# Performance work log

Measured on AMD Instinct MI355X. Metric: run time of the kernel, lower is better.

Reference implementation:

```python
import jax, jax.numpy as jnp
import numpy as np

N, E = 50000, 1600000
D_IN, D_OUT = 256, 64
ALPHA = 0.2        # LeakyReLU slope used on attention logits (self.leakyrelu)
BT_SLOPE = 0.01    # F.leaky_relu default slope inside relu_bt


def _xavier_normal(key, shape, gain):
    fan_in, fan_out = shape[0], shape[1]
    std = gain * np.sqrt(2.0 / (fan_in + fan_out))
    return jax.random.normal(key, shape, dtype=jnp.float32) * std


def relu_bt(x):
    # -threshold(-leaky_relu(x), -t, -t) == min(leaky_relu(x), t), t = ||x||_inf (detached)
    t = jax.lax.stop_gradient(jnp.max(jnp.abs(x)))
    y = jnp.where(x >= 0, x, BT_SLOPE * x)
    return jnp.minimum(y, t)


def setup_inputs() -> dict:
    key = jax.random.key(0)
    k0, k1, k2, k3, k4, k5 = jax.random.split(key, 6)
    inp = jax.random.normal(k0, (N, D_IN), dtype=jnp.float32)
    edge = jax.random.randint(k1, (2, E), 0, N, dtype=jnp.int64)
    W_high = _xavier_normal(k2, (D_IN, D_OUT), 1.414)
    W_low = _xavier_normal(k3, (D_IN, D_OUT), 1.414)
    a_high = _xavier_normal(k4, (1, D_OUT), 1.414)
    a_low = _xavier_normal(k5, (1, D_OUT), 1.414)
    return {"input": inp, "edge": edge, "W_high": W_high, "W_low": W_low,
            "a_high": a_high, "a_low": a_low}


def reference(input, edge, W_high, W_low, a_high, a_low):
    n = input.shape[0]
    src, dst = edge[0], edge[1]

    h_high = relu_bt(input @ W_high)  # [N, D_OUT]
    h_low = relu_bt(input @ W_low)    # [N, D_OUT]

    # a @ (h[src] -/+ h[dst])^T == (a.h)[src] -/+ (a.h)[dst]: compute per-node scalar
    # projections first, then gather scalars per edge (avoids [E, D_OUT] edge features).
    s_high = h_high @ a_high[0]       # [N]
    s_low = h_low @ a_low[0]          # [N]

    def lrelu(x):
        return jnp.where(x >= 0, x, ALPHA * x)

    edge_e_high = jnp.exp(-lrelu(s_high[src] - s_high[dst]))  # [E]
    edge_e_low = jnp.exp(-lrelu(s_low[src] + s_low[dst]))     # [E]
    # dropout p=0.0 -> identity

    # sparse A @ ones -> per-row sum of attention weights
    rowsum_high = jax.ops.segment_sum(edge_e_high, src, num_segments=n)[:, None]
    rowsum_low = jax.ops.segment_sum(edge_e_low, src, num_segments=n)[:, None]

    # sparse A @ h -> weighted aggregation of neighbor features
    hp_high = jax.ops.segment_sum(edge_e_high[:, None] * h_high[dst], src, num_segments=n)
    hp_low = jax.ops.segment_sum(edge_e_low[:, None] * h_low[dst], src, num_segments=n)

    hp_high = hp_high / (rowsum_high + 1e-16)
    hp_low = hp_low / (rowsum_low + 1e-16)

    # concat=True branch
    return relu_bt(jnp.concatenate([hp_high, hp_low], axis=1))  # [N, 2*D_OUT]
```

## Files before the change

### kernel.cpp

```cpp
#include <hip/hip_runtime.h>
#include <hip/hip_bf16.h>
#include <cstdint>

#define NN    50000
#define NE    1600000
#define DIN   256
#define DOUT  64
#define CAPS  96
#define CAPD  95

#define BKT   196
#define BCAP  10240
#define EPB   4096
#define EPT   16
#define NBIN  391
#define MTB   64
#define NGEMM 782
#define CSPL  4

typedef __attribute__((ext_vector_type(8))) short frag8;
typedef __attribute__((ext_vector_type(4))) float fragc;

union PK { __hip_bfloat162 b2; uint32_t u; };
union CH { frag8 v; uint32_t u[4]; };

__device__ __forceinline__ float leaky01(float x) { return x >= 0.f ? x : 0.01f * x; }

__device__ __forceinline__ uint32_t pk2(float lo, float hi) {
  PK p; p.b2 = __float22bfloat162_rn(make_float2(lo, hi)); return p.u;
}

__device__ __forceinline__ int   bcast_i(int v, int lane) {
  return __builtin_amdgcn_readlane(v, lane);
}
__device__ __forceinline__ float bcast_f(float v, int lane) {
  return __int_as_float(__builtin_amdgcn_readlane(__float_as_int(v), lane));
}

__device__ __forceinline__ float bfH(uint32_t u) { return __uint_as_float(u << 16); }
__device__ __forceinline__ float bfL(uint32_t u) { return __uint_as_float(u & 0xffff0000u); }

__global__ __launch_bounds__(256) void prep_kernel(
    const float* __restrict__ Wh, const float* __restrict__ Wl,
    __hip_bfloat16* __restrict__ Wt, int* __restrict__ cursor)
{
  if (blockIdx.x == 0 && threadIdx.x < BKT) cursor[threadIdx.x] = 0;
  int g = blockIdx.x * 256 + threadIdx.x;
  if (g < 2 * DOUT * DIN) {
    int m = g >> 14, rem = g & 16383;
    int n = rem >> 8, k = rem & 255;
    float v = (m ? Wl : Wh)[k * DOUT + n];
    Wt[g] = __float2bfloat16(v);
  }
}

__global__ __launch_bounds__(256) void fused_kernel(
    const float* __restrict__ inp, const __hip_bfloat16* __restrict__ Wt,
    const float* __restrict__ ah, const float* __restrict__ al,
    const int* __restrict__ edge, int* __restrict__ cursor,
    uint32_t* __restrict__ binned, uint32_t* __restrict__ HL,
    float2* __restrict__ ss)
{
  __shared__ __align__(16) char smem[32768];

  const int idx = blockIdx.x;
  const int t = threadIdx.x;

  if (idx < NBIN) {
    uint32_t* stage  = (uint32_t*)smem;
    int*      hist   = (int*)(smem + 16384);
    int*      cur    = (int*)(smem + 17408);
    int*      base_g = (int*)(smem + 18192);
    int*      scan_s = (int*)(smem + 18976);

    const int e0 = idx * EPB;
    uint32_t v[EPT];
#pragma unroll
    for (int i = 0; i < EPT; i++) {
      int e = e0 + i * 256 + t;
      if (e < NE) {
        uint32_t s = (uint32_t)edge[e];
        uint32_t d = (uint32_t)edge[NE + e];
        v[i] = (s << 16) | d;
      } else {
        v[i] = 0xFFFFFFFFu;
      }
    }
    if (t < 256) hist[t] = 0;
    for (int b = t; b < BKT; b += 256) cur[b] = 0;
    __syncthreads();
#pragma unroll
    for (int i = 0; i < EPT; i++) {
      int b = v[i] >> 24;
      if (b < BKT) atomicAdd(&hist[b], 1);
    }
    __syncthreads();
    if (t < 64) {
      int carry = 0;
#pragma unroll
      for (int seg = 0; seg < 4; seg++) {
        int i = seg * 64 + t;
        int h = hist[i];
        int s = h;
#pragma unroll
        for (int off = 1; off < 64; off <<= 1) {
          int o = __shfl_up(s, off);
          if (t >= off) s += o;
        }
        int excl = carry + s - h;
        if (i <= BKT) scan_s[i] = excl;
        carry += bcast_i(s, 63);
      }
    }
    __syncthreads();
    for (int b = t; b < BKT; b += 256) {
      int h = hist[b];
      base_g[b] = h ? atomicAdd(&cursor[b], h) : 0;
    }
    __syncthreads();
#pragma unroll
    for (int i = 0; i < EPT; i++) {
      int b = v[i] >> 24;
      if (b < BKT) {
        int pos = atomicAdd(&cur[b], 1);
        stage[scan_s[b] + pos] = v[i];
      }
    }
    __syncthreads();
    const int total = scan_s[BKT];
    for (int i = t; i < total; i += 256) {
      uint32_t sv = stage[i];
      int bb = sv >> 24;
      int ofs = base_g[bb] + (i - scan_s[bb]);
      if (ofs < BCAP) binned[(size_t)bb * BCAP + ofs] = sv;
    }
    return;
  }

  frag8* asmem = (frag8*)smem;
  const int gid = idx - NBIN;
  const int n0 = gid * MTB;
  const int lane = t & 63;
  const int w = t >> 6;
  const int quad = lane >> 4, nn = lane & 15;

  const frag8* Wt8 = (const frag8*)Wt;
  const int bbase = ((w * 16 + nn) << 5) + quad;
  frag8 bH[8], bL[8];
#pragma unroll
  for (int q = 0; q < 8; q++) {
    bH[q] = Wt8[bbase + (q << 2)];
    bL[q] = Wt8[2048 + bbase + (q << 2)];
  }

  const float4* inp4 = (const float4*)inp;
#pragma unroll
  for (int i = 0; i < 8; i++) {
    int c = i * 256 + t;
    int r = c & 15;
    int cc = c >> 4;
    int qd = cc & 3;
    int wq = cc >> 2;
    int row = ((wq >> 3) << 4) + r;
    int k0 = ((wq & 7) << 5) + (qd << 3);
    int node = n0 + row;
    float4 a0 = make_float4(0.f, 0.f, 0.f, 0.f), a1 = a0;
    if (node < NN) {
      a0 = inp4[(size_t)node * 64 + (k0 >> 2)];
      a1 = inp4[(size_t)node * 64 + (k0 >> 2) + 1];
    }
    CH ch;
    ch.u[0] = pk2(a0.x, a0.y);
    ch.u[1] = pk2(a0.z, a0.w);
    ch.u[2] = pk2(a1.x, a1.y);
    ch.u[3] = pk2(a1.z, a1.w);
    asmem[c] = ch.v;
  }
  __syncthreads();

  fragc accH[4], accL[4];
#pragma unroll
  for (int m = 0; m < 4; m++) {
    accH[m] = (fragc){0.f, 0.f, 0.f, 0.f};
    accL[m] = (fragc){0.f, 0.f, 0.f, 0.f};
  }

#pragma unroll
  for (int q = 0; q < 8; q++) {
#pragma unroll
    for (int mt = 0; mt < 4; mt++) {
      frag8 af = asmem[(mt << 9) + (q << 6) + lane];
      accH[mt] = __builtin_amdgcn_mfma_f32_16x16x32_bf16(af, bH[q], accH[mt], 0, 0, 0);
      accL[mt] = __builtin_amdgcn_mfma_f32_16x16x32_bf16(af, bL[q], accL[mt], 0, 0, 0);
    }
  }
  __syncthreads();

  float* sred = (float*)smem;
  const float ahv = ah[w * 16 + nn];
  const float alv = al[w * 16 + nn];
#pragma unroll
  for (int mt = 0; mt < 4; mt++) {
#pragma unroll
    for (int r = 0; r < 4; r++) {
      int rowb = (mt << 4) + (quad << 2) + r;
      int node = n0 + rowb;
      float hH = leaky01(accH[mt][r]);
      float hL = leaky01(accL[mt][r]);
      if (node < NN) HL[(size_t)node * DOUT + w * 16 + nn] = pk2(hH, hL);
      float pH = hH * ahv, pL = hL * alv;
#pragma unroll
      for (int off = 1; off < 16; off <<= 1) {
        pH += __shfl_xor(pH, off);
        pL += __shfl_xor(pL, off);
      }
      if (nn == 0) {
        sred[rowb * 8 + w]     = pH;
        sred[rowb * 8 + 4 + w] = pL;
      }
    }
  }
  __syncthreads();
  if (t < 64) {
    int node = n0 + t;
    if (node < NN) {
      float sH = sred[t * 8 + 0] + sred[t * 8 + 1] + sred[t * 8 + 2] + sred[t * 8 + 3];
      float sL = sred[t * 8 + 4] + sred[t * 8 + 5] + sred[t * 8 + 6] + sred[t * 8 + 7];
      ss[node] = make_float2(sH, sL);
    }
  }
}

__global__ __launch_bounds__(256) void csr_kernel(
    const uint32_t* __restrict__ binned, const int* __restrict__ cursor,
    int* __restrict__ col)
{
  __shared__ int lst[64][CAPS];
  __shared__ int cnt[64];
  const int b    = blockIdx.x / CSPL;
  const int part = blockIdx.x % CSPL;
  const int t = threadIdx.x;
  if (t < 64) cnt[t] = 0;
  __syncthreads();
  int n = cursor[b]; if (n > BCAP) n = BCAP;
  const uint32_t* eb = binned + (size_t)b * BCAP;
  for (int i = t; i < n; i += 256) {
    uint32_t v = eb[i];
    int src = v >> 16, dst = v & 0xffff;
    int loc = src & 255;
    if ((loc >> 6) == part) {
      int pos = atomicAdd(&cnt[loc & 63], 1);
      if (pos < CAPD) lst[loc & 63][1 + pos] = dst;
    }
  }
  __syncthreads();
  if (t < 64) {
    int c = cnt[t]; if (c > CAPD) c = CAPD;
    lst[t][0] = c;
  }
  __syncthreads();
  const int base_node = (b << 8) + (part << 6);
  int4* dst4 = (int4*)(col + (size_t)base_node * CAPS);
  const int4* src4 = (const int4*)&lst[0][0];
  for (int i = t; i < 64 * CAPS / 4; i += 256) {
    int node = base_node + i / (CAPS / 4);
    if (node < NN) dst4[i] = src4[i];
  }
}

__global__ __launch_bounds__(256) void agg_kernel(
    const uint32_t* __restrict__ HL, const float2* __restrict__ ss,
    const int* __restrict__ col, float* __restrict__ out)
{
  int wave = (blockIdx.x * blockDim.x + threadIdx.x) >> 6;
  int lane = threadIdx.x & 63;
  if (wave >= NN) return;
  const int n = wave;
  const int* cl = col + (size_t)n * CAPS;
  int d = cl[0]; if (d > CAPD) d = CAPD;

  const float2 sn = ss[n];

  float accH = 0.f, accL = 0.f, rsH = 0.f, rsL = 0.f;

  for (int base = 0; base < d; base += 64) {
    int m = d - base; if (m > 64) m = 64;
    int   dst_l = 0;
    float eh_l = 0.f, el_l = 0.f;
    if (lane < m) {
      dst_l = cl[1 + base + lane];
      float2 sd = ss[dst_l];
      float xh = sn.x - sd.x;
      xh = (xh >= 0.f) ? xh : 0.2f * xh;
      eh_l = __expf(-xh);
      float xl = sn.y + sd.y;
      xl = (xl >= 0.f) ? xl : 0.2f * xl;
      el_l = __expf(-xl);
    }
    int j = 0;
    for (; j + 8 <= m; j += 8) {
      uint32_t u[8]; float eh[8], el[8];
#pragma unroll
      for (int x = 0; x < 8; x++) {
        int dd = bcast_i(dst_l, j + x);
        u[x]  = HL[((uint32_t)dd << 6) + lane];
        eh[x] = bcast_f(eh_l, j + x);
        el[x] = bcast_f(el_l, j + x);
      }
#pragma unroll
      for (int x = 0; x < 8; x++) {
        accH += eh[x] * bfH(u[x]); accL += el[x] * bfL(u[x]);
        rsH += eh[x]; rsL += el[x];
      }
    }
    for (; j < m; j++) {
      int      dst = bcast_i(dst_l, j);
      float    eh  = bcast_f(eh_l, j);
      float    el  = bcast_f(el_l, j);
      uint32_t u   = HL[((uint32_t)dst << 6) + lane];
      accH += eh * bfH(u);
      accL += el * bfL(u);
      rsH += eh;
      rsL += el;
    }
  }

  float oh = accH / (rsH + 1e-16f);
  float ol = accL / (rsL + 1e-16f);
  out[(size_t)n * 128 + lane]      = leaky01(oh);
  out[(size_t)n * 128 + 64 + lane] = leaky01(ol);
}

extern "C" void kernel_launch(void* const* d_in, const int* in_sizes, int n_in,
                              void* d_out, int out_size, void* d_ws, size_t ws_size,
                              hipStream_t stream) {
  const float* inp  = (const float*)d_in[0];
  const int*   edge = (const int*)d_in[1];
  const float* Wh   = (const float*)d_in[2];
  const float* Wl   = (const float*)d_in[3];
  const float* ah   = (const float*)d_in[4];
  const float* al   = (const float*)d_in[5];
  float* out = (float*)d_out;

  char* ws = (char*)d_ws;
  uint32_t* HL     = (uint32_t*)(ws + 0);
  float2*   ss     = (float2*)  (ws + 12800000);
  int*      col    = (int*)     (ws + 13200000);
  uint32_t* binned = (uint32_t*)(ws + 32400000);
  int*      cursor = (int*)     (ws + 40428160);
  __hip_bfloat16* Wt = (__hip_bfloat16*)(ws + 13200000);

  prep_kernel<<<128, 256, 0, stream>>>(Wh, Wl, Wt, cursor);
  fused_kernel<<<NBIN + NGEMM, 256, 0, stream>>>(inp, Wt, ah, al, edge,
                                                 cursor, binned, HL, ss);
  csr_kernel<<<BKT * CSPL, 256, 0, stream>>>(binned, cursor, col);
  agg_kernel<<<NN / 4, 256, 0, stream>>>(HL, ss, col, out);
}
```

Baseline: 198.0 us.

## Split agg wave into half-waves gathering two edges per step with 8-byte loads

The aggregation loop now has each half of the wave handle a different neighbour edge at the same time: the lower half takes even edges, the upper half takes odd edges. Each lane loads a uint2 of packed bf16 features, so a half-wave covers a full 64-column row. Edge indices and weights are broadcast with ds_bpermute instead of readlane. Row sums are computed with a butterfly shuffle reduction rather than per-edge accumulation, and the two halves' partial sums are combined with a final xor-32 shuffle before a float2 store. The aim is to halve the serial gather iterations and widen each memory request, at the cost of extra cross-lane shuffles and some wasted slots when the degree is small.

```diff
diff --git a/kernel.cpp b/kernel.cpp
--- a/kernel.cpp
+++ b/kernel.cpp
@@ -32,9 +32,6 @@
 
 __device__ __forceinline__ int   bcast_i(int v, int lane) {
   return __builtin_amdgcn_readlane(v, lane);
-}
-__device__ __forceinline__ float bcast_f(float v, int lane) {
-  return __int_as_float(__builtin_amdgcn_readlane(__float_as_int(v), lane));
 }
 
 __device__ __forceinline__ float bfH(uint32_t u) { return __uint_as_float(u << 16); }
@@ -280,8 +277,13 @@
   int d = cl[0]; if (d > CAPD) d = CAPD;
 
   const float2 sn = ss[n];
-
-  float accH = 0.f, accL = 0.f, rsH = 0.f, rsL = 0.f;
+  const uint2* HL2 = (const uint2*)HL;
+
+  const int vodd4 = (lane & 32) >> 3;
+  const int lo31  = lane & 31;
+
+  float accH0 = 0.f, accH1 = 0.f, accL0 = 0.f, accL1 = 0.f;
+  float rsH = 0.f, rsL = 0.f;
 
   for (int base = 0; base < d; base += 64) {
     int m = d - base; if (m > 64) m = 64;
@@ -297,38 +299,51 @@
       xl = (xl >= 0.f) ? xl : 0.2f * xl;
       el_l = __expf(-xl);
     }
-    int j = 0;
-    for (; j + 8 <= m; j += 8) {
-      uint32_t u[8]; float eh[8], el[8];
-#pragma unroll
-      for (int x = 0; x < 8; x++) {
-        int dd = bcast_i(dst_l, j + x);
-        u[x]  = HL[((uint32_t)dd << 6) + lane];
-        eh[x] = bcast_f(eh_l, j + x);
-        el[x] = bcast_f(el_l, j + x);
-      }
-#pragma unroll
-      for (int x = 0; x < 8; x++) {
-        accH += eh[x] * bfH(u[x]); accL += el[x] * bfL(u[x]);
-        rsH += eh[x]; rsL += el[x];
-      }
-    }
-    for (; j < m; j++) {
-      int      dst = bcast_i(dst_l, j);
-      float    eh  = bcast_f(eh_l, j);
-      float    el  = bcast_f(el_l, j);
-      uint32_t u   = HL[((uint32_t)dst << 6) + lane];
-      accH += eh * bfH(u);
-      accL += el * bfL(u);
-      rsH += eh;
-      rsL += el;
-    }
-  }
-
-  float oh = accH / (rsH + 1e-16f);
-  float ol = accL / (rsL + 1e-16f);
-  out[(size_t)n * 128 + lane]      = leaky01(oh);
-  out[(size_t)n * 128 + 64 + lane] = leaky01(ol);
+    const int ehb = __float_as_int(eh_l);
+    const int elb = __float_as_int(el_l);
+    const int pj = (m + 1) >> 1;
+    for (int jj = 0; jj < pj; jj += 4) {
+      int vdd[4]; float veh[4], vel[4]; uint2 u[4];
+#pragma unroll
+      for (int x = 0; x < 4; x++) {
+        int ib = vodd4 + ((jj + x) << 3);
+        vdd[x] = __builtin_amdgcn_ds_bpermute(ib, dst_l);
+        veh[x] = __int_as_float(__builtin_amdgcn_ds_bpermute(ib, ehb));
+        vel[x] = __int_as_float(__builtin_amdgcn_ds_bpermute(ib, elb));
+      }
+#pragma unroll
+      for (int x = 0; x < 4; x++)
+        u[x] = HL2[(((uint32_t)vdd[x]) << 5) + lo31];
+#pragma unroll
+      for (int x = 0; x < 4; x++) {
+        accH0 += veh[x] * bfH(u[x].x);
+        accL0 += vel[x] * bfL(u[x].x);
+        accH1 += veh[x] * bfH(u[x].y);
+        accL1 += vel[x] * bfL(u[x].y);
+      }
+    }
+    float rh = eh_l, rl = el_l;
+#pragma unroll
+    for (int off = 1; off < 64; off <<= 1) {
+      rh += __shfl_xor(rh, off);
+      rl += __shfl_xor(rl, off);
+    }
+    rsH += rh; rsL += rl;
+  }
+
+  accH0 += __shfl_xor(accH0, 32);
+  accH1 += __shfl_xor(accH1, 32);
+  accL0 += __shfl_xor(accL0, 32);
+  accL1 += __shfl_xor(accL1, 32);
+
+  float r  = (lane < 32) ? rsH : rsL;
+  float a0 = (lane < 32) ? accH0 : accL0;
+  float a1 = (lane < 32) ? accH1 : accL1;
+  float inv = 1.f / (r + 1e-16f);
+  float o0 = leaky01(a0 * inv);
+  float o1 = leaky01(a1 * inv);
+  float2* op = (float2*)(out + (size_t)n * 128 + ((lane & 32) << 1) + (lo31 << 1));
+  *op = make_float2(o0, o1);
 }
 
 extern "C" void kernel_launch(void* const* d_in, const int* in_sizes, int n_in,
```

Result: no change. 197.0 us (-0.5%).
